# Performance work log

Hardware: AMD Instinct MI355X
Metric: run time of the kernel (lower is better)

Reference implementation:

```python
import jax, jax.numpy as jnp
import numpy as np

B, S, E = 2, 2048, 2048
H, HKV, KQV = 16, 4, 2048
D = KQV // H            # 128 head dim
KV_DIM = D * HKV        # 512
WINDOW = 256
NEG = jnp.finfo(jnp.float32).min


def setup_inputs() -> dict:
    key = jax.random.key(0)
    ks = jax.random.split(key, 5)
    sc = 0.02
    return {
        "hidden_states": jax.random.normal(ks[0], (B, S, E), jnp.float32),
        "Wq": jax.random.normal(ks[1], (KQV, E), jnp.float32) * sc,
        "Wk": jax.random.normal(ks[2], (KV_DIM, E), jnp.float32) * sc,
        "Wv": jax.random.normal(ks[3], (KV_DIM, E), jnp.float32) * sc,
        "Wo": jax.random.normal(ks[4], (E, KQV), jnp.float32) * sc,
        "bo": jnp.zeros((E,), jnp.float32),
    }


def reference(hidden_states, Wq, Wk, Wv, Wo, bo):
    x = hidden_states
    # projections (nn.Linear: x @ W.T)
    q = (x @ Wq.T).reshape(B, S, H, D).transpose(0, 2, 1, 3)      # [B,H,S,D]
    k = (x @ Wk.T).reshape(B, S, HKV, D).transpose(0, 2, 1, 3)    # [B,HKV,S,D]
    v = (x @ Wv.T).reshape(B, S, HKV, D).transpose(0, 2, 1, 3)

    # faithful reproduction of the module's index_select head expansion:
    # group_sizes are uniform (H % HKV == 0); both query and kv indices are
    # [0]*g + [1]*g + ... so query head i (i < HKV) is duplicated g times.
    idx = jnp.repeat(jnp.arange(HKV), H // HKV)                   # [H]
    qs = q[:, idx]                                                # [B,H,S,D]
    ks = k[:, idx]
    vs = v[:, idx]

    # GPT-Neo style: no 1/sqrt(D) scaling
    scores = jnp.einsum('bhqd,bhkd->bhqk', qs, ks)                # [B,H,S,S]

    i = jnp.arange(S)[:, None]
    j = jnp.arange(S)[None, :]
    # local causal mask: j <= i and j > i - WINDOW
    mask = (j <= i) & (j > i - WINDOW)                            # [S,S]
    scores = jnp.where(mask[None, None], scores, NEG)
    attn = jax.nn.softmax(scores, axis=-1)

    out = jnp.einsum('bhqk,bhkd->bhqd', attn, vs)                 # [B,H,S,D]
    out = out.transpose(0, 2, 1, 3).reshape(B, S, H * D)          # merge heads
    return out @ Wo.T + bo
```

## Files before the change

### kernel.cpp

```cpp
#include <hip/hip_runtime.h>

typedef _Float16 f16;
typedef _Float16 f16x8 __attribute__((ext_vector_type(8)));
typedef _Float16 f16x4 __attribute__((ext_vector_type(4)));
typedef float    f32x4 __attribute__((ext_vector_type(4)));


__device__ __forceinline__ void load_lds16(const void* g, void* l) {
    __builtin_amdgcn_global_load_lds(
        (__attribute__((address_space(1))) void*)(g),
        (__attribute__((address_space(3))) void*)(l), 16, 0, 0);
}

__global__ __launch_bounds__(256)
void cvt_fold(const float* __restrict__ X, const float* __restrict__ Wq,
              const float* __restrict__ Wk, const float* __restrict__ Wv,
              const float* __restrict__ Wo,
              f16* __restrict__ Xh, f16* __restrict__ Wqh,
              f16* __restrict__ Wkh, f16* __restrict__ Wvh, f16* __restrict__ Wr)
{
    int blk = blockIdx.x;
    if (blk < 11264) {
        size_t o = ((size_t)blk * 256 + threadIdx.x) * 4;
        const float* src; f16* dst; size_t off;
        if (o < 8388608)       { src = X;  dst = Xh;  off = o; }
        else if (o < 9437184)  { src = Wq; dst = Wqh; off = o - 8388608; }
        else if (o < 10485760) { src = Wk; dst = Wkh; off = o - 9437184; }
        else                   { src = Wv; dst = Wvh; off = o - 10485760; }
        float4 v = *(const float4*)(src + off);
        f16x4 b;
        b[0] = (f16)v.x; b[1] = (f16)v.y; b[2] = (f16)v.z; b[3] = (f16)v.w;
        *(f16x4*)(dst + off) = b;
    } else {
        size_t t = (size_t)(blk - 11264) * 256 + threadIdx.x;
        size_t o = t * 4;
        int e = (int)(o >> 9);
        int c = (int)(o & 511);
        int g = c >> 7, d0 = c & 127;
        const float* src = Wo + (size_t)e * 2048 + g * 512 + d0;
        float4 a0 = *(const float4*)(src);
        float4 a1 = *(const float4*)(src + 128);
        float4 a2 = *(const float4*)(src + 256);
        float4 a3 = *(const float4*)(src + 384);
        f16x4 ob;
        ob[0] = (f16)(a0.x + a1.x + a2.x + a3.x);
        ob[1] = (f16)(a0.y + a1.y + a2.y + a3.y);
        ob[2] = (f16)(a0.z + a1.z + a2.z + a3.z);
        ob[3] = (f16)(a0.w + a1.w + a2.w + a3.w);
        *(f16x4*)(Wr + o) = ob;
    }
}

__global__ __launch_bounds__(256)
void qkv_gemm(const f16* __restrict__ X, const f16* __restrict__ Wq,
              const f16* __restrict__ Wk, const f16* __restrict__ Wv,
              f16* __restrict__ Qo, f16* __restrict__ Ko, f16* __restrict__ Vo)
{
    const int z = blockIdx.z;
    const f16* Bw = (z == 0) ? Wq : (z == 1) ? Wk : Wv;
    f16* C = (z == 0) ? Qo : (z == 1) ? Ko : Vo;
    const int K = 2048;

    __shared__ __align__(16) f16 As[128 * 32];
    __shared__ __align__(16) f16 Bs[128 * 32];

    const int tid = threadIdx.x;
    const int wave = tid >> 6, lane = tid & 63;
    const int lrow = lane & 15, lquad = lane >> 4;
    const int wr = wave >> 1, wc = wave & 1;
    const int m0 = blockIdx.y * 128, n0 = blockIdx.x * 128;

    f32x4 acc[4][4];
    const f32x4 z4 = {0.f, 0.f, 0.f, 0.f};
    for (int i = 0; i < 4; i++) for (int j = 0; j < 4; j++) acc[i][j] = z4;

    for (int k0 = 0; k0 < K; k0 += 32) {
        __syncthreads();
        for (int i = 0; i < 2; i++) {
            int sb = i * 256 + wave * 64;
            int slot = sb + lane;
            int row = slot >> 2, kc = slot & 3;
            load_lds16(X  + (size_t)(m0 + row) * K + k0 + kc * 8, As + sb * 8);
            load_lds16(Bw + (size_t)(n0 + row) * K + k0 + kc * 8, Bs + sb * 8);
        }
        __syncthreads();
        f16x8 af[4], bfr[4];
        for (int mt = 0; mt < 4; mt++)
            af[mt]  = *(const f16x8*)(As + (wr * 64 + mt * 16 + lrow) * 32 + lquad * 8);
        for (int nt = 0; nt < 4; nt++)
            bfr[nt] = *(const f16x8*)(Bs + (wc * 64 + nt * 16 + lrow) * 32 + lquad * 8);
        for (int mt = 0; mt < 4; mt++)
            for (int nt = 0; nt < 4; nt++)
                acc[mt][nt] = __builtin_amdgcn_mfma_f32_16x16x32_f16(af[mt], bfr[nt], acc[mt][nt], 0, 0, 0);
    }

    if (z < 2) {
        for (int mt = 0; mt < 4; mt++) {
            int mbase = m0 + wr * 64 + mt * 16 + lquad * 4;
            for (int r = 0; r < 4; r++) {
                int m = mbase + r;
                int b = m >> 11, s = m & 2047;
                for (int nt = 0; nt < 4; nt++) {
                    int n = n0 + wc * 64 + nt * 16 + lrow;
                    int h = n >> 7, d = n & 127;
                    C[(size_t)(((b * 4 + h) << 11) + s) * 128 + d] = (f16)acc[mt][nt][r];
                }
            }
        }
    } else {
        for (int mt = 0; mt < 4; mt++) {
            int mbase = m0 + wr * 64 + mt * 16 + lquad * 4;
            int b = mbase >> 11, s = mbase & 2047;
            for (int nt = 0; nt < 4; nt++) {
                int n = n0 + wc * 64 + nt * 16 + lrow;
                int h = n >> 7, d = n & 127;
                f16x4 pk;
                for (int r = 0; r < 4; r++) pk[r] = (f16)acc[mt][nt][r];
                *(f16x4*)(C + ((size_t)((b * 4 + h) * 128 + d) << 11) + s) = pk;
            }
        }
    }
}

__global__ __launch_bounds__(64)
void attn_win(const f16* __restrict__ Q, const f16* __restrict__ Kc,
              const f16* __restrict__ Vt, f16* __restrict__ AO)
{
    const int bg = blockIdx.y;
    const int b = bg >> 2, g = bg & 3;
    const int qbase = blockIdx.x * 16;
    const int lane = threadIdx.x;
    const int lrow = lane & 15, lquad = lane >> 4;

    const f16* Qb = Q  + (size_t)(b * 4 + g) * (2048 * 128);
    const f16* Kb = Kc + (size_t)(b * 4 + g) * (2048 * 128);
    const f16* Vb = Vt + (size_t)(b * 4 + g) * (128 * 2048);

    __shared__ __align__(16) f16 Pl[16 * 128];

    f16x8 qf[4];
    for (int ks = 0; ks < 4; ks++)
        qf[ks] = *(const f16x8*)(Qb + (size_t)(qbase + lrow) * 128 + ks * 32 + lquad * 8);

    float m_i[4], l_i[4];
    f32x4 oa[8];
    const f32x4 z4 = {0.f, 0.f, 0.f, 0.f};
    for (int r = 0; r < 4; r++) { m_i[r] = -30000.f; l_i[r] = 0.f; }
    for (int nt = 0; nt < 8; nt++) oa[nt] = z4;

    const int t0 = (qbase >= 256) ? (((qbase - 255) >> 7) << 7) : 0;
    for (int kt = t0; kt <= qbase + 15; kt += 128) {
        f32x4 sc[8];
        for (int nt = 0; nt < 8; nt++) sc[nt] = z4;
        for (int nt = 0; nt < 8; nt++) {
            for (int ks = 0; ks < 4; ks++) {
                f16x8 kf = *(const f16x8*)(Kb + (size_t)(kt + nt * 16 + lrow) * 128 + ks * 32 + lquad * 8);
                sc[nt] = __builtin_amdgcn_mfma_f32_16x16x32_f16(qf[ks], kf, sc[nt], 0, 0, 0);
            }
        }
        for (int r = 0; r < 4; r++) {
            const int qi = qbase + lquad * 4 + r;
            float rmax = -60000.f;
            for (int nt = 0; nt < 8; nt++) {
                int kj = kt + nt * 16 + lrow;
                float sval = sc[nt][r];
                bool ok = (kj <= qi) && (kj + 256 > qi);
                sval = ok ? sval : -60000.f;
                sc[nt][r] = sval;
                rmax = fmaxf(rmax, sval);
            }
            rmax = fmaxf(rmax, __shfl_xor(rmax, 1));
            rmax = fmaxf(rmax, __shfl_xor(rmax, 2));
            rmax = fmaxf(rmax, __shfl_xor(rmax, 4));
            rmax = fmaxf(rmax, __shfl_xor(rmax, 8));
            float mold = m_i[r];
            float mnew = fmaxf(mold, rmax);
            float alpha = __expf(mold - mnew);
            m_i[r] = mnew;
            float rsum = 0.f;
            for (int nt = 0; nt < 8; nt++) {
                float p = __expf(sc[nt][r] - mnew);
                sc[nt][r] = p;
                rsum += p;
            }
            rsum += __shfl_xor(rsum, 1);
            rsum += __shfl_xor(rsum, 2);
            rsum += __shfl_xor(rsum, 4);
            rsum += __shfl_xor(rsum, 8);
            l_i[r] = l_i[r] * alpha + rsum;
            for (int nt = 0; nt < 8; nt++) oa[nt][r] *= alpha;
        }
        for (int nt = 0; nt < 8; nt++)
            for (int r = 0; r < 4; r++)
                Pl[(lquad * 4 + r) * 128 + nt * 16 + lrow] = (f16)sc[nt][r];
        __syncthreads();
        f16x8 pf[4];
        for (int ks = 0; ks < 4; ks++)
            pf[ks] = *(const f16x8*)(Pl + lrow * 128 + ks * 32 + lquad * 8);
        for (int nt = 0; nt < 8; nt++) {
            for (int ks = 0; ks < 4; ks++) {
                f16x8 vf = *(const f16x8*)(Vb + (size_t)(nt * 16 + lrow) * 2048 + kt + ks * 32 + lquad * 8);
                oa[nt] = __builtin_amdgcn_mfma_f32_16x16x32_f16(pf[ks], vf, oa[nt], 0, 0, 0);
            }
        }
        __syncthreads();
    }
    float inv[4];
    for (int r = 0; r < 4; r++) inv[r] = (l_i[r] > 0.f) ? 1.f / l_i[r] : 0.f;
    for (int nt = 0; nt < 8; nt++) {
        for (int r = 0; r < 4; r++) {
            int q = qbase + lquad * 4 + r;
            int d = nt * 16 + lrow;
            AO[(size_t)(b * 2048 + q) * 512 + g * 128 + d] = (f16)(oa[nt][r] * inv[r]);
        }
    }
}

__global__ __launch_bounds__(256)
void out_gemm(const f16* __restrict__ A, const f16* __restrict__ Bw,
              const float* __restrict__ bias, float* __restrict__ C)
{
    const int K = 512, N = 2048;
    __shared__ __align__(16) f16 As[128 * 32];
    __shared__ __align__(16) f16 Bs[128 * 32];

    const int tid = threadIdx.x;
    const int wave = tid >> 6, lane = tid & 63;
    const int lrow = lane & 15, lquad = lane >> 4;
    const int wr = wave >> 1, wc = wave & 1;
    const int m0 = blockIdx.y * 128, n0 = blockIdx.x * 128;

    f32x4 acc[4][4];
    const f32x4 z4 = {0.f, 0.f, 0.f, 0.f};
    for (int i = 0; i < 4; i++) for (int j = 0; j < 4; j++) acc[i][j] = z4;

    for (int k0 = 0; k0 < K; k0 += 32) {
        __syncthreads();
        for (int i = 0; i < 2; i++) {
            int sb = i * 256 + wave * 64;
            int slot = sb + lane;
            int row = slot >> 2, kc = slot & 3;
            load_lds16(A  + (size_t)(m0 + row) * K + k0 + kc * 8, As + sb * 8);
            load_lds16(Bw + (size_t)(n0 + row) * K + k0 + kc * 8, Bs + sb * 8);
        }
        __syncthreads();
        f16x8 af[4], bfr[4];
        for (int mt = 0; mt < 4; mt++)
            af[mt]  = *(const f16x8*)(As + (wr * 64 + mt * 16 + lrow) * 32 + lquad * 8);
        for (int nt = 0; nt < 4; nt++)
            bfr[nt] = *(const f16x8*)(Bs + (wc * 64 + nt * 16 + lrow) * 32 + lquad * 8);
        for (int mt = 0; mt < 4; mt++)
            for (int nt = 0; nt < 4; nt++)
                acc[mt][nt] = __builtin_amdgcn_mfma_f32_16x16x32_f16(af[mt], bfr[nt], acc[mt][nt], 0, 0, 0);
    }

    for (int nt = 0; nt < 4; nt++) {
        int n = n0 + wc * 64 + nt * 16 + lrow;
        float bv2 = bias[n];
        for (int mt = 0; mt < 4; mt++) {
            int mbase = m0 + wr * 64 + mt * 16 + lquad * 4;
            for (int r = 0; r < 4; r++)
                C[(size_t)(mbase + r) * N + n] = acc[mt][nt][r] + bv2;
        }
    }
}

extern "C" void kernel_launch(void* const* d_in, const int* in_sizes, int n_in,
                              void* d_out, int out_size, void* d_ws, size_t ws_size,
                              hipStream_t stream)
{
    const float* x  = (const float*)d_in[0];
    const float* Wq = (const float*)d_in[1];
    const float* Wk = (const float*)d_in[2];
    const float* Wv = (const float*)d_in[3];
    const float* Wo = (const float*)d_in[4];
    const float* bo = (const float*)d_in[5];
    float* out = (float*)d_out;

    f16* Xh  = (f16*)d_ws;
    f16* AO  = Xh;
    f16* Wqh = Xh  + 8388608;
    f16* Wkh = Wqh + 1048576;
    f16* Wvh = Wkh + 1048576;
    f16* Wr  = Wvh + 1048576;
    f16* Qws = Wr  + 1048576;
    f16* Kws = Qws + 2097152;
    f16* Vws = Kws + 2097152;

    cvt_fold<<<dim3(12288), 256, 0, stream>>>(x, Wq, Wk, Wv, Wo, Xh, Wqh, Wkh, Wvh, Wr);
    qkv_gemm<<<dim3(4, 32, 3), 256, 0, stream>>>(Xh, Wqh, Wkh, Wvh, Qws, Kws, Vws);
    attn_win<<<dim3(128, 8), 64, 0, stream>>>(Qws, Kws, Vws, AO);
    out_gemm<<<dim3(16, 32), 256, 0, stream>>>(AO, Wr, bo, out);
}
```

Measured before the change: 215.7 us.

## Double-buffer LDS tiles and XOR-swizzle layout in QKV and output GEMMs

Both the QKV projection GEMM and the output GEMM now keep two LDS buffers, so the global-to-LDS load of the next K tile is issued before the MFMAs on the current tile. This replaces the two barriers per iteration with one. The LDS layout is also XOR-swizzled on the 16-byte chunk index, both on the global source side and in the fragment reads, to cut bank conflicts. LDS use doubles, which may lower occupancy. The single barrier relies on the async global_load_lds finishing before that barrier, and correctness depends on this.

Result: no change. 216.3 us (+0.3%).

```diff
diff --git a/kernel.cpp b/kernel.cpp
--- a/kernel.cpp
+++ b/kernel.cpp
@@ -61,8 +61,8 @@
     f16* C = (z == 0) ? Qo : (z == 1) ? Ko : Vo;
     const int K = 2048;
 
-    __shared__ __align__(16) f16 As[128 * 32];
-    __shared__ __align__(16) f16 Bs[128 * 32];
+    __shared__ __align__(16) f16 As[2][128 * 32];
+    __shared__ __align__(16) f16 Bs[2][128 * 32];
 
     const int tid = threadIdx.x;
     const int wave = tid >> 6, lane = tid & 63;
@@ -70,28 +70,54 @@
     const int wr = wave >> 1, wc = wave & 1;
     const int m0 = blockIdx.y * 128, n0 = blockIdx.x * 128;
 
+    const int sb0 = wave * 64;
+    const int sb1 = 256 + wave * 64;
+    const int row0 = (sb0 + lane) >> 2, kc0 = (sb0 + lane) & 3;
+    const int row1 = (sb1 + lane) >> 2, kc1 = (sb1 + lane) & 3;
+    const int kcs0 = kc0 ^ ((row0 >> 1) & 3);
+    const int kcs1 = kc1 ^ ((row1 >> 1) & 3);
+    const f16* a_src0 = X  + (size_t)(m0 + row0) * K + kcs0 * 8;
+    const f16* b_src0 = Bw + (size_t)(n0 + row0) * K + kcs0 * 8;
+    const f16* a_src1 = X  + (size_t)(m0 + row1) * K + kcs1 * 8;
+    const f16* b_src1 = Bw + (size_t)(n0 + row1) * K + kcs1 * 8;
+
     f32x4 acc[4][4];
     const f32x4 z4 = {0.f, 0.f, 0.f, 0.f};
     for (int i = 0; i < 4; i++) for (int j = 0; j < 4; j++) acc[i][j] = z4;
 
+    load_lds16(a_src0, &As[0][sb0 * 8]);
+    load_lds16(b_src0, &Bs[0][sb0 * 8]);
+    load_lds16(a_src1, &As[0][sb1 * 8]);
+    load_lds16(b_src1, &Bs[0][sb1 * 8]);
+    __syncthreads();
+
+    int aoff[4], boff[4];
+    for (int t = 0; t < 4; t++) {
+        int ra = wr * 64 + t * 16 + lrow;
+        aoff[t] = ra * 32 + ((lquad ^ ((ra >> 1) & 3)) << 3);
+        int rb = wc * 64 + t * 16 + lrow;
+        boff[t] = rb * 32 + ((lquad ^ ((rb >> 1) & 3)) << 3);
+    }
+
+    int cur = 0;
     for (int k0 = 0; k0 < K; k0 += 32) {
-        __syncthreads();
-        for (int i = 0; i < 2; i++) {
-            int sb = i * 256 + wave * 64;
-            int slot = sb + lane;
-            int row = slot >> 2, kc = slot & 3;
-            load_lds16(X  + (size_t)(m0 + row) * K + k0 + kc * 8, As + sb * 8);
-            load_lds16(Bw + (size_t)(n0 + row) * K + k0 + kc * 8, Bs + sb * 8);
-        }
-        __syncthreads();
+        if (k0 + 32 < K) {
+            int nxt = cur ^ 1;
+            load_lds16(a_src0 + k0 + 32, &As[nxt][sb0 * 8]);
+            load_lds16(b_src0 + k0 + 32, &Bs[nxt][sb0 * 8]);
+            load_lds16(a_src1 + k0 + 32, &As[nxt][sb1 * 8]);
+            load_lds16(b_src1 + k0 + 32, &Bs[nxt][sb1 * 8]);
+        }
         f16x8 af[4], bfr[4];
         for (int mt = 0; mt < 4; mt++)
-            af[mt]  = *(const f16x8*)(As + (wr * 64 + mt * 16 + lrow) * 32 + lquad * 8);
+            af[mt]  = *(const f16x8*)(&As[cur][aoff[mt]]);
         for (int nt = 0; nt < 4; nt++)
-            bfr[nt] = *(const f16x8*)(Bs + (wc * 64 + nt * 16 + lrow) * 32 + lquad * 8);
+            bfr[nt] = *(const f16x8*)(&Bs[cur][boff[nt]]);
         for (int mt = 0; mt < 4; mt++)
             for (int nt = 0; nt < 4; nt++)
                 acc[mt][nt] = __builtin_amdgcn_mfma_f32_16x16x32_f16(af[mt], bfr[nt], acc[mt][nt], 0, 0, 0);
+        __syncthreads();
+        cur ^= 1;
     }
 
     if (z < 2) {
@@ -221,8 +247,8 @@
               const float* __restrict__ bias, float* __restrict__ C)
 {
     const int K = 512, N = 2048;
-    __shared__ __align__(16) f16 As[128 * 32];
-    __shared__ __align__(16) f16 Bs[128 * 32];
+    __shared__ __align__(16) f16 As[2][128 * 32];
+    __shared__ __align__(16) f16 Bs[2][128 * 32];
 
     const int tid = threadIdx.x;
     const int wave = tid >> 6, lane = tid & 63;
@@ -230,28 +256,54 @@
     const int wr = wave >> 1, wc = wave & 1;
     const int m0 = blockIdx.y * 128, n0 = blockIdx.x * 128;
 
+    const int sb0 = wave * 64;
+    const int sb1 = 256 + wave * 64;
+    const int row0 = (sb0 + lane) >> 2, kc0 = (sb0 + lane) & 3;
+    const int row1 = (sb1 + lane) >> 2, kc1 = (sb1 + lane) & 3;
+    const int kcs0 = kc0 ^ ((row0 >> 1) & 3);
+    const int kcs1 = kc1 ^ ((row1 >> 1) & 3);
+    const f16* a_src0 = A  + (size_t)(m0 + row0) * K + kcs0 * 8;
+    const f16* b_src0 = Bw + (size_t)(n0 + row0) * K + kcs0 * 8;
+    const f16* a_src1 = A  + (size_t)(m0 + row1) * K + kcs1 * 8;
+    const f16* b_src1 = Bw + (size_t)(n0 + row1) * K + kcs1 * 8;
+
     f32x4 acc[4][4];
     const f32x4 z4 = {0.f, 0.f, 0.f, 0.f};
     for (int i = 0; i < 4; i++) for (int j = 0; j < 4; j++) acc[i][j] = z4;
 
+    load_lds16(a_src0, &As[0][sb0 * 8]);
+    load_lds16(b_src0, &Bs[0][sb0 * 8]);
+    load_lds16(a_src1, &As[0][sb1 * 8]);
+    load_lds16(b_src1, &Bs[0][sb1 * 8]);
+    __syncthreads();
+
+    int aoff[4], boff[4];
+    for (int t = 0; t < 4; t++) {
+        int ra = wr * 64 + t * 16 + lrow;
+        aoff[t] = ra * 32 + ((lquad ^ ((ra >> 1) & 3)) << 3);
+        int rb = wc * 64 + t * 16 + lrow;
+        boff[t] = rb * 32 + ((lquad ^ ((rb >> 1) & 3)) << 3);
+    }
+
+    int cur = 0;
     for (int k0 = 0; k0 < K; k0 += 32) {
-        __syncthreads();
-        for (int i = 0; i < 2; i++) {
-            int sb = i * 256 + wave * 64;
-            int slot = sb + lane;
-            int row = slot >> 2, kc = slot & 3;
-            load_lds16(A  + (size_t)(m0 + row) * K + k0 + kc * 8, As + sb * 8);
-            load_lds16(Bw + (size_t)(n0 + row) * K + k0 + kc * 8, Bs + sb * 8);
-        }
-        __syncthreads();
+        if (k0 + 32 < K) {
+            int nxt = cur ^ 1;
+            load_lds16(a_src0 + k0 + 32, &As[nxt][sb0 * 8]);
+            load_lds16(b_src0 + k0 + 32, &Bs[nxt][sb0 * 8]);
+            load_lds16(a_src1 + k0 + 32, &As[nxt][sb1 * 8]);
+            load_lds16(b_src1 + k0 + 32, &Bs[nxt][sb1 * 8]);
+        }
         f16x8 af[4], bfr[4];
         for (int mt = 0; mt < 4; mt++)
-            af[mt]  = *(const f16x8*)(As + (wr * 64 + mt * 16 + lrow) * 32 + lquad * 8);
+            af[mt]  = *(const f16x8*)(&As[cur][aoff[mt]]);
         for (int nt = 0; nt < 4; nt++)
-            bfr[nt] = *(const f16x8*)(Bs + (wc * 64 + nt * 16 + lrow) * 32 + lquad * 8);
+            bfr[nt] = *(const f16x8*)(&Bs[cur][boff[nt]]);
         for (int mt = 0; mt < 4; mt++)
             for (int nt = 0; nt < 4; nt++)
                 acc[mt][nt] = __builtin_amdgcn_mfma_f32_16x16x32_f16(af[mt], bfr[nt], acc[mt][nt], 0, 0, 0);
+        __syncthreads();
+        cur ^= 1;
     }
 
     for (int nt = 0; nt < 4; nt++) {
```

## Triple-buffer GEMM LDS loads with swizzle and smaller M tiles

Applied to the files above, without the earlier changes.

Both the QKV and output GEMMs now use a three-stage LDS ring filled by direct global-to-LDS loads, so the next two K-steps are in flight while the current one computes, with one barrier per step instead of two. The LDS layout gets an XOR swizzle on the 16-byte chunk index to reduce bank conflicts on fragment reads. The M tile is halved to 64 rows and the grid doubled, which gives more blocks for occupancy but less reuse of each loaded B tile. Hand-written waitcnt counts must match the three loads issued per stage.

Measured after the change: 220.1 us. 1.02x slower.

```diff
diff --git a/kernel.cpp b/kernel.cpp
--- a/kernel.cpp
+++ b/kernel.cpp
@@ -51,6 +51,13 @@
     }
 }
 
+#define STAGE3(t, buf)                                          \
+    {                                                           \
+        load_lds16(gsrc0 + (t) * 32, &S[buf][loff0]);           \
+        load_lds16(gsrc1 + (t) * 32, &S[buf][loff1]);           \
+        load_lds16(gsrc2 + (t) * 32, &S[buf][loff2]);           \
+    }
+
 __global__ __launch_bounds__(256)
 void qkv_gemm(const f16* __restrict__ X, const f16* __restrict__ Wq,
               const f16* __restrict__ Wk, const f16* __restrict__ Wv,
@@ -60,46 +67,90 @@
     const f16* Bw = (z == 0) ? Wq : (z == 1) ? Wk : Wv;
     f16* C = (z == 0) ? Qo : (z == 1) ? Ko : Vo;
     const int K = 2048;
-
-    __shared__ __align__(16) f16 As[128 * 32];
-    __shared__ __align__(16) f16 Bs[128 * 32];
+    const int NSTEP = 64;
+
+    __shared__ __align__(16) f16 S[3][6144];
 
     const int tid = threadIdx.x;
     const int wave = tid >> 6, lane = tid & 63;
     const int lrow = lane & 15, lquad = lane >> 4;
     const int wr = wave >> 1, wc = wave & 1;
-    const int m0 = blockIdx.y * 128, n0 = blockIdx.x * 128;
-
-    f32x4 acc[4][4];
+    const int m0 = blockIdx.y * 64, n0 = blockIdx.x * 128;
+
+    const f16* gsrc0; const f16* gsrc1; const f16* gsrc2;
+    int loff0, loff1, loff2;
+    {
+        int s;
+        s = (wave * 3 + 0) * 64 + lane;
+        { int isB = s >= 256; int s2 = isB ? s - 256 : s; int row = s2 >> 2, kc = s2 & 3;
+          int kcs = kc ^ ((row >> 1) & 3); loff0 = s * 8;
+          gsrc0 = (isB ? Bw + (size_t)(n0 + row) * K : X + (size_t)(m0 + row) * K) + kcs * 8; }
+        s = (wave * 3 + 1) * 64 + lane;
+        { int isB = s >= 256; int s2 = isB ? s - 256 : s; int row = s2 >> 2, kc = s2 & 3;
+          int kcs = kc ^ ((row >> 1) & 3); loff1 = s * 8;
+          gsrc1 = (isB ? Bw + (size_t)(n0 + row) * K : X + (size_t)(m0 + row) * K) + kcs * 8; }
+        s = (wave * 3 + 2) * 64 + lane;
+        { int isB = s >= 256; int s2 = isB ? s - 256 : s; int row = s2 >> 2, kc = s2 & 3;
+          int kcs = kc ^ ((row >> 1) & 3); loff2 = s * 8;
+          gsrc2 = (isB ? Bw + (size_t)(n0 + row) * K : X + (size_t)(m0 + row) * K) + kcs * 8; }
+    }
+
+    int aoff[2], boff[4];
+#pragma unroll
+    for (int t = 0; t < 2; t++) {
+        int ra = wr * 32 + t * 16 + lrow;
+        aoff[t] = ra * 32 + ((lquad ^ ((ra >> 1) & 3)) << 3);
+    }
+#pragma unroll
+    for (int t = 0; t < 4; t++) {
+        int rb = wc * 64 + t * 16 + lrow;
+        boff[t] = 2048 + rb * 32 + ((lquad ^ ((rb >> 1) & 3)) << 3);
+    }
+
+    f32x4 acc[2][4];
     const f32x4 z4 = {0.f, 0.f, 0.f, 0.f};
-    for (int i = 0; i < 4; i++) for (int j = 0; j < 4; j++) acc[i][j] = z4;
-
-    for (int k0 = 0; k0 < K; k0 += 32) {
-        __syncthreads();
-        for (int i = 0; i < 2; i++) {
-            int sb = i * 256 + wave * 64;
-            int slot = sb + lane;
-            int row = slot >> 2, kc = slot & 3;
-            load_lds16(X  + (size_t)(m0 + row) * K + k0 + kc * 8, As + sb * 8);
-            load_lds16(Bw + (size_t)(n0 + row) * K + k0 + kc * 8, Bs + sb * 8);
-        }
-        __syncthreads();
-        f16x8 af[4], bfr[4];
-        for (int mt = 0; mt < 4; mt++)
-            af[mt]  = *(const f16x8*)(As + (wr * 64 + mt * 16 + lrow) * 32 + lquad * 8);
-        for (int nt = 0; nt < 4; nt++)
-            bfr[nt] = *(const f16x8*)(Bs + (wc * 64 + nt * 16 + lrow) * 32 + lquad * 8);
-        for (int mt = 0; mt < 4; mt++)
+#pragma unroll
+    for (int i = 0; i < 2; i++) for (int j = 0; j < 4; j++) acc[i][j] = z4;
+
+    STAGE3(0, 0);
+    STAGE3(1, 1);
+
+    int buf = 0;
+    for (int t = 0; t < NSTEP; ++t) {
+        if (t < NSTEP - 2) {
+            asm volatile("s_waitcnt vmcnt(3) lgkmcnt(0)" ::: "memory");
+            __builtin_amdgcn_s_barrier();
+            int nb = buf + 2; if (nb >= 3) nb -= 3;
+            STAGE3(t + 2, nb);
+        } else if (t == NSTEP - 2) {
+            asm volatile("s_waitcnt vmcnt(3) lgkmcnt(0)" ::: "memory");
+            __builtin_amdgcn_s_barrier();
+        } else {
+            asm volatile("s_waitcnt vmcnt(0) lgkmcnt(0)" ::: "memory");
+            __builtin_amdgcn_s_barrier();
+        }
+        f16x8 af[2], bf[4];
+#pragma unroll
+        for (int mt = 0; mt < 2; mt++) af[mt] = *(const f16x8*)(&S[buf][aoff[mt]]);
+#pragma unroll
+        for (int nt = 0; nt < 4; nt++) bf[nt] = *(const f16x8*)(&S[buf][boff[nt]]);
+#pragma unroll
+        for (int mt = 0; mt < 2; mt++)
+#pragma unroll
             for (int nt = 0; nt < 4; nt++)
-                acc[mt][nt] = __builtin_amdgcn_mfma_f32_16x16x32_f16(af[mt], bfr[nt], acc[mt][nt], 0, 0, 0);
+                acc[mt][nt] = __builtin_amdgcn_mfma_f32_16x16x32_f16(af[mt], bf[nt], acc[mt][nt], 0, 0, 0);
+        buf += 1; if (buf == 3) buf = 0;
     }
 
     if (z < 2) {
-        for (int mt = 0; mt < 4; mt++) {
-            int mbase = m0 + wr * 64 + mt * 16 + lquad * 4;
+#pragma unroll
+        for (int mt = 0; mt < 2; mt++) {
+            int mbase = m0 + wr * 32 + mt * 16 + lquad * 4;
+#pragma unroll
             for (int r = 0; r < 4; r++) {
                 int m = mbase + r;
                 int b = m >> 11, s = m & 2047;
+#pragma unroll
                 for (int nt = 0; nt < 4; nt++) {
                     int n = n0 + wc * 64 + nt * 16 + lrow;
                     int h = n >> 7, d = n & 127;
@@ -108,13 +159,16 @@
             }
         }
     } else {
-        for (int mt = 0; mt < 4; mt++) {
-            int mbase = m0 + wr * 64 + mt * 16 + lquad * 4;
+#pragma unroll
+        for (int mt = 0; mt < 2; mt++) {
+            int mbase = m0 + wr * 32 + mt * 16 + lquad * 4;
             int b = mbase >> 11, s = mbase & 2047;
+#pragma unroll
             for (int nt = 0; nt < 4; nt++) {
                 int n = n0 + wc * 64 + nt * 16 + lrow;
                 int h = n >> 7, d = n & 127;
                 f16x4 pk;
+#pragma unroll
                 for (int r = 0; r < 4; r++) pk[r] = (f16)acc[mt][nt][r];
                 *(f16x4*)(C + ((size_t)((b * 4 + h) * 128 + d) << 11) + s) = pk;
             }
@@ -221,44 +275,89 @@
               const float* __restrict__ bias, float* __restrict__ C)
 {
     const int K = 512, N = 2048;
-    __shared__ __align__(16) f16 As[128 * 32];
-    __shared__ __align__(16) f16 Bs[128 * 32];
+    const int NSTEP = 16;
+
+    __shared__ __align__(16) f16 S[3][6144];
 
     const int tid = threadIdx.x;
     const int wave = tid >> 6, lane = tid & 63;
     const int lrow = lane & 15, lquad = lane >> 4;
     const int wr = wave >> 1, wc = wave & 1;
-    const int m0 = blockIdx.y * 128, n0 = blockIdx.x * 128;
-
-    f32x4 acc[4][4];
+    const int m0 = blockIdx.y * 64, n0 = blockIdx.x * 128;
+
+    const f16* gsrc0; const f16* gsrc1; const f16* gsrc2;
+    int loff0, loff1, loff2;
+    {
+        int s;
+        s = (wave * 3 + 0) * 64 + lane;
+        { int isB = s >= 256; int s2 = isB ? s - 256 : s; int row = s2 >> 2, kc = s2 & 3;
+          int kcs = kc ^ ((row >> 1) & 3); loff0 = s * 8;
+          gsrc0 = (isB ? Bw + (size_t)(n0 + row) * K : A + (size_t)(m0 + row) * K) + kcs * 8; }
+        s = (wave * 3 + 1) * 64 + lane;
+        { int isB = s >= 256; int s2 = isB ? s - 256 : s; int row = s2 >> 2, kc = s2 & 3;
+          int kcs = kc ^ ((row >> 1) & 3); loff1 = s * 8;
+          gsrc1 = (isB ? Bw + (size_t)(n0 + row) * K : A + (size_t)(m0 + row) * K) + kcs * 8; }
+        s = (wave * 3 + 2) * 64 + lane;
+        { int isB = s >= 256; int s2 = isB ? s - 256 : s; int row = s2 >> 2, kc = s2 & 3;
+          int kcs = kc ^ ((row >> 1) & 3); loff2 = s * 8;
+          gsrc2 = (isB ? Bw + (size_t)(n0 + row) * K : A + (size_t)(m0 + row) * K) + kcs * 8; }
+    }
+
+    int aoff[2], boff[4];
+#pragma unroll
+    for (int t = 0; t < 2; t++) {
+        int ra = wr * 32 + t * 16 + lrow;
+        aoff[t] = ra * 32 + ((lquad ^ ((ra >> 1) & 3)) << 3);
+    }
+#pragma unroll
+    for (int t = 0; t < 4; t++) {
+        int rb = wc * 64 + t * 16 + lrow;
+        boff[t] = 2048 + rb * 32 + ((lquad ^ ((rb >> 1) & 3)) << 3);
+    }
+
+    f32x4 acc[2][4];
     const f32x4 z4 = {0.f, 0.f, 0.f, 0.f};
-    for (int i = 0; i < 4; i++) for (int j = 0; j < 4; j++) acc[i][j] = z4;
-
-    for (int k0 = 0; k0 < K; k0 += 32) {
-        __syncthreads();
-        for (int i = 0; i < 2; i++) {
-            int sb = i * 256 + wave * 64;
-            int slot = sb + lane;
-            int row = slot >> 2, kc = slot & 3;
-            load_lds16(A  + (size_t)(m0 + row) * K + k0 + kc * 8, As + sb * 8);
-            load_lds16(Bw + (size_t)(n0 + row) * K + k0 + kc * 8, Bs + sb * 8);
-        }
-        __syncthreads();
-        f16x8 af[4], bfr[4];
-        for (int mt = 0; mt < 4; mt++)
-            af[mt]  = *(const f16x8*)(As + (wr * 64 + mt * 16 + lrow) * 32 + lquad * 8);
-        for (int nt = 0; nt < 4; nt++)
-            bfr[nt] = *(const f16x8*)(Bs + (wc * 64 + nt * 16 + lrow) * 32 + lquad * 8);
-        for (int mt = 0; mt < 4; mt++)
+#pragma unroll
+    for (int i = 0; i < 2; i++) for (int j = 0; j < 4; j++) acc[i][j] = z4;
+
+    STAGE3(0, 0);
+    STAGE3(1, 1);
+
+    int buf = 0;
+    for (int t = 0; t < NSTEP; ++t) {
+        if (t < NSTEP - 2) {
+            asm volatile("s_waitcnt vmcnt(3) lgkmcnt(0)" ::: "memory");
+            __builtin_amdgcn_s_barrier();
+            int nb = buf + 2; if (nb >= 3) nb -= 3;
+            STAGE3(t + 2, nb);
+        } else if (t == NSTEP - 2) {
+            asm volatile("s_waitcnt vmcnt(3) lgkmcnt(0)" ::: "memory");
+            __builtin_amdgcn_s_barrier();
+        } else {
+            asm volatile("s_waitcnt vmcnt(0) lgkmcnt(0)" ::: "memory");
+            __builtin_amdgcn_s_barrier();
+        }
+        f16x8 af[2], bf[4];
+#pragma unroll
+        for (int mt = 0; mt < 2; mt++) af[mt] = *(const f16x8*)(&S[buf][aoff[mt]]);
+#pragma unroll
+        for (int nt = 0; nt < 4; nt++) bf[nt] = *(const f16x8*)(&S[buf][boff[nt]]);
+#pragma unroll
+        for (int mt = 0; mt < 2; mt++)
+#pragma unroll
             for (int nt = 0; nt < 4; nt++)
-                acc[mt][nt] = __builtin_amdgcn_mfma_f32_16x16x32_f16(af[mt], bfr[nt], acc[mt][nt], 0, 0, 0);
-    }
-
+                acc[mt][nt] = __builtin_amdgcn_mfma_f32_16x16x32_f16(af[mt], bf[nt], acc[mt][nt], 0, 0, 0);
+        buf += 1; if (buf == 3) buf = 0;
+    }
+
+#pragma unroll
     for (int nt = 0; nt < 4; nt++) {
         int n = n0 + wc * 64 + nt * 16 + lrow;
         float bv2 = bias[n];
-        for (int mt = 0; mt < 4; mt++) {
-            int mbase = m0 + wr * 64 + mt * 16 + lquad * 4;
+#pragma unroll
+        for (int mt = 0; mt < 2; mt++) {
+            int mbase = m0 + wr * 32 + mt * 16 + lquad * 4;
+#pragma unroll
             for (int r = 0; r < 4; r++)
                 C[(size_t)(mbase + r) * N + n] = acc[mt][nt][r] + bv2;
         }
@@ -288,7 +387,7 @@
     f16* Vws = Kws + 2097152;
 
     cvt_fold<<<dim3(12288), 256, 0, stream>>>(x, Wq, Wk, Wv, Wo, Xh, Wqh, Wkh, Wvh, Wr);
-    qkv_gemm<<<dim3(4, 32, 3), 256, 0, stream>>>(Xh, Wqh, Wkh, Wvh, Qws, Kws, Vws);
+    qkv_gemm<<<dim3(4, 64, 3), 256, 0, stream>>>(Xh, Wqh, Wkh, Wvh, Qws, Kws, Vws);
     attn_win<<<dim3(128, 8), 64, 0, stream>>>(Qws, Kws, Vws, AO);
-    out_gemm<<<dim3(16, 32), 256, 0, stream>>>(AO, Wr, bo, out);
-}
+    out_gemm<<<dim3(16, 64), 256, 0, stream>>>(AO, Wr, bo, out);
+}
```
